# Optimization experiments

Measured on AMD Instinct MI355X. Metric: run time of the kernel, lower is better.

Reference implementation:

```python
import jax, jax.numpy as jnp
import numpy as np

B, S, E, H = 4, 1024, 1024, 16
HD = E // H  # head_dim = 64


def setup_inputs() -> dict:
    key = jax.random.key(0)
    ks = jax.random.split(key, 7)
    return {
        "query": jax.random.normal(ks[0], (B, S, E), dtype=jnp.float32),
        "key": jax.random.normal(ks[1], (B, S, E), dtype=jnp.float32),
        "value": jax.random.normal(ks[2], (B, S, E), dtype=jnp.float32),
        # per-head Linear weights stacked: [H, head_dim, emb_dim] (torch Linear is y = x @ W^T)
        "Wq": jax.random.normal(ks[3], (H, HD, E), dtype=jnp.float32) * (E ** -0.5),
        "Wk": jax.random.normal(ks[4], (H, HD, E), dtype=jnp.float32) * (E ** -0.5),
        "Wv": jax.random.normal(ks[5], (H, HD, E), dtype=jnp.float32) * (E ** -0.5),
        "Wo": jax.random.normal(ks[6], (E, E), dtype=jnp.float32) * (E ** -0.5),
    }


def reference(query, key, value, Wq, Wk, Wv, Wo):
    # Project per head (all heads vectorized): [B,S,E] x [H,HD,E] -> [B,H,S,HD]
    Q = jnp.einsum('bse,hde->bhsd', query, Wq)
    K = jnp.einsum('bse,hde->bhsd', key, Wk)
    V = jnp.einsum('bse,hde->bhsd', value, Wv)
    scale = 1.0 / np.sqrt(HD)  # source divides by sqrt(emb_dim / n_head)
    scores = jnp.einsum('bhsd,bhtd->bhst', Q, K) * scale  # [B,H,S,S]
    p = jax.nn.softmax(scores, axis=-1)
    ctx = jnp.einsum('bhst,bhtd->bhsd', p, V)  # [B,H,S,HD]
    # concat heads along feature dim -> [B,S,E]
    concat = ctx.transpose(0, 2, 1, 3).reshape(query.shape[0], query.shape[1], -1)
    return concat @ Wo.T
```

## Files before the change

### kernel.cpp

```cpp
#include <hip/hip_runtime.h>

typedef __bf16 bf16_t;
typedef __bf16 bf16x4 __attribute__((ext_vector_type(4)));
typedef __bf16 bf16x8 __attribute__((ext_vector_type(8)));
typedef float f32x4 __attribute__((ext_vector_type(4)));
typedef short short4v __attribute__((ext_vector_type(4)));

#define E_DIM 1024
#define S_LEN 1024
#define NHEAD 16
#define HD_DIM 64
#define BATCH 4
#define TOKENS 4096

__device__ __forceinline__ void async_copy16(const bf16_t* g, bf16_t* l) {
    __builtin_amdgcn_global_load_lds((const __attribute__((address_space(1))) void*)g,
                                     (__attribute__((address_space(3))) void*)l,
                                     16, 0, 0);
}

__device__ __forceinline__ f32x4 pv_mfma(bf16x4 a, bf16x4 b, f32x4 c) {
#if __has_builtin(__builtin_amdgcn_mfma_f32_16x16x16_bf16)
    return __builtin_amdgcn_mfma_f32_16x16x16_bf16(a, b, c, 0, 0, 0);
#elif __has_builtin(__builtin_amdgcn_mfma_f32_16x16x16bf16_1k)
    short4v as, bs;
    __builtin_memcpy(&as, &a, 8);
    __builtin_memcpy(&bs, &b, 8);
    return __builtin_amdgcn_mfma_f32_16x16x16bf16_1k(as, bs, c, 0, 0, 0);
#else
    f32x4 d;
    asm volatile("v_mfma_f32_16x16x16_bf16 %0, %1, %2, %3\n\ts_nop 7\n\ts_nop 7"
                 : "=v"(d)
                 : "v"(a), "v"(b), "v"(c));
    return d;
#endif
}

__device__ __forceinline__ void stage_tiles(const bf16_t* gA, const bf16_t* gB,
                                            bf16_t* sAbuf, bf16_t* sBbuf,
                                            int wave, int k0) {
    const int K = 1024;
#pragma unroll
    for (int cc = 0; cc < 4; cc++) {
        int c = wave * 4 + cc;
        if (c < 8)
            async_copy16(gA + (size_t)c * 16 * K + k0, sAbuf + c * 16 * 32);
        else
            async_copy16(gB + (size_t)(c - 8) * 16 * K + k0, sBbuf + (c - 8) * 16 * 32);
    }
}

__global__ __launch_bounds__(256) void cast_all(const float* __restrict__ q,
                                                const float* __restrict__ k,
                                                const float* __restrict__ v,
                                                const float* __restrict__ wq,
                                                const float* __restrict__ wk,
                                                const float* __restrict__ wv,
                                                const float* __restrict__ wo,
                                                bf16_t* __restrict__ dst) {
    const size_t NX = (size_t)TOKENS * E_DIM;
    const size_t NW = (size_t)E_DIM * E_DIM;
    size_t i = ((size_t)blockIdx.x * 256 + threadIdx.x) * 8;
    const float* src;
    size_t off;
    if (i < 3 * NX) {
        int a = (int)(i >> 22);
        src = a == 0 ? q : (a == 1 ? k : v);
        off = i & (NX - 1);
    } else {
        size_t j = i - 3 * NX;
        int a = (int)(j >> 20);
        src = a == 0 ? wq : (a == 1 ? wk : (a == 2 ? wv : wo));
        off = j & (NW - 1);
    }
    float4 x = *(const float4*)(src + off);
    float4 y = *(const float4*)(src + off + 4);
    bf16x8 o;
    o[0] = (bf16_t)x.x; o[1] = (bf16_t)x.y; o[2] = (bf16_t)x.z; o[3] = (bf16_t)x.w;
    o[4] = (bf16_t)y.x; o[5] = (bf16_t)y.y; o[6] = (bf16_t)y.z; o[7] = (bf16_t)y.w;
    *(bf16x8*)(dst + i) = o;
}

__global__ __launch_bounds__(256, 4) void proj_gemm(const bf16_t* __restrict__ Xq,
                                                    const bf16_t* __restrict__ Xk,
                                                    const bf16_t* __restrict__ Xv,
                                                    const bf16_t* __restrict__ Wq,
                                                    const bf16_t* __restrict__ Wk,
                                                    const bf16_t* __restrict__ Wv,
                                                    bf16_t* __restrict__ Qp,
                                                    bf16_t* __restrict__ Kp,
                                                    bf16_t* __restrict__ Vp) {
    __shared__ bf16_t sA[2][128 * 32];
    __shared__ bf16_t sB[2][128 * 32];
    const int z = blockIdx.z;
    const bf16_t* A = z == 0 ? Xq : (z == 1 ? Xk : Xv);
    const bf16_t* B = z == 0 ? Wq : (z == 1 ? Wk : Wv);
    bf16_t* C = z == 0 ? Qp : (z == 1 ? Kp : Vp);
    const int N = 1024, K = 1024;
    const int lid = blockIdx.x + 8 * blockIdx.y;
    const int m0 = (((lid & 7) << 2) + ((lid >> 3) & 3)) * 128;
    const int n0 = (lid >> 5) * 128;

    const int tid = threadIdx.x;
    const int wave = tid >> 6, lane = tid & 63;
    const int quad = lane >> 4, l16 = lane & 15;
    const int wm = (wave >> 1) * 64, wn = (wave & 1) * 64;
    const int srow = lane >> 2, scol = (lane & 3) * 8;

    const bf16_t* gA = A + (size_t)(m0 + srow) * K + scol;
    const bf16_t* gB = B + (size_t)(n0 + srow) * K + scol;

    f32x4 acc[4][4];
    const f32x4 vzero = {0.f, 0.f, 0.f, 0.f};
#pragma unroll
    for (int mt = 0; mt < 4; mt++)
#pragma unroll
        for (int nt = 0; nt < 4; nt++) acc[mt][nt] = vzero;

#define PROJ_COMPUTE(cur)                                                             \
    {                                                                                 \
        bf16x8 af[4], bfr[4];                                                         \
        _Pragma("unroll") for (int mt = 0; mt < 4; mt++)                              \
            af[mt] = *(const bf16x8*)&sA[cur][(wm + mt * 16 + l16) * 32 + quad * 8];  \
        _Pragma("unroll") for (int nt = 0; nt < 4; nt++)                              \
            bfr[nt] = *(const bf16x8*)&sB[cur][(wn + nt * 16 + l16) * 32 + quad * 8]; \
        _Pragma("unroll") for (int mt = 0; mt < 4; mt++)                              \
            _Pragma("unroll") for (int nt = 0; nt < 4; nt++)                          \
                acc[mt][nt] = __builtin_amdgcn_mfma_f32_16x16x32_bf16(                \
                    af[mt], bfr[nt], acc[mt][nt], 0, 0, 0);                           \
    }

    stage_tiles(gA, gB, sA[0], sB[0], wave, 0);
    stage_tiles(gA, gB, sA[1], sB[1], wave, 32);

    int cur = 0;
#pragma unroll 1
    for (int it = 0; it < 31; ++it) {
        asm volatile("s_waitcnt vmcnt(4)" ::: "memory");
        asm volatile("s_barrier" ::: "memory");
        PROJ_COMPUTE(cur);
        asm volatile("s_waitcnt lgkmcnt(0)" ::: "memory");
        asm volatile("s_barrier" ::: "memory");
        int knext = (it + 2) * 32;
        if (knext < K) stage_tiles(gA, gB, sA[cur], sB[cur], wave, knext);
        cur ^= 1;
    }
    asm volatile("s_waitcnt vmcnt(0)" ::: "memory");
    asm volatile("s_barrier" ::: "memory");
    PROJ_COMPUTE(cur);
#undef PROJ_COMPUTE

#pragma unroll
    for (int mt = 0; mt < 4; mt++)
#pragma unroll
        for (int nt = 0; nt < 4; nt++)
#pragma unroll
            for (int r = 0; r < 4; r++) {
                int row = m0 + wm + mt * 16 + quad * 4 + r;
                int col = n0 + wn + nt * 16 + l16;
                C[(size_t)row * N + col] = (bf16_t)acc[mt][nt][r];
            }
}

__global__ __launch_bounds__(256, 4) void out_gemm(const bf16_t* __restrict__ A,
                                                   const bf16_t* __restrict__ B,
                                                   float* __restrict__ C) {
    __shared__ bf16_t sA[2][128 * 32];
    __shared__ bf16_t sB[2][128 * 32];
    const int N = 1024, K = 1024;
    const int lid = blockIdx.x + 8 * blockIdx.y;
    const int m0 = (((lid & 7) << 2) + ((lid >> 3) & 3)) * 128;
    const int n0 = (lid >> 5) * 128;

    const int tid = threadIdx.x;
    const int wave = tid >> 6, lane = tid & 63;
    const int quad = lane >> 4, l16 = lane & 15;
    const int wm = (wave >> 1) * 64, wn = (wave & 1) * 64;
    const int srow = lane >> 2, scol = (lane & 3) * 8;

    const bf16_t* gA = A + (size_t)(m0 + srow) * K + scol;
    const bf16_t* gB = B + (size_t)(n0 + srow) * K + scol;

    f32x4 acc[4][4];
    const f32x4 vzero = {0.f, 0.f, 0.f, 0.f};
#pragma unroll
    for (int mt = 0; mt < 4; mt++)
#pragma unroll
        for (int nt = 0; nt < 4; nt++) acc[mt][nt] = vzero;

    stage_tiles(gA, gB, sA[0], sB[0], wave, 0);
    asm volatile("s_waitcnt vmcnt(0)" ::: "memory");
    __syncthreads();

    int cur = 0;
    for (int k0 = 32; k0 < K; k0 += 32) {
        stage_tiles(gA, gB, sA[cur ^ 1], sB[cur ^ 1], wave, k0);

        bf16x8 af[4], bfr[4];
#pragma unroll
        for (int mt = 0; mt < 4; mt++)
            af[mt] = *(const bf16x8*)&sA[cur][(wm + mt * 16 + l16) * 32 + quad * 8];
#pragma unroll
        for (int nt = 0; nt < 4; nt++)
            bfr[nt] = *(const bf16x8*)&sB[cur][(wn + nt * 16 + l16) * 32 + quad * 8];
#pragma unroll
        for (int mt = 0; mt < 4; mt++)
#pragma unroll
            for (int nt = 0; nt < 4; nt++)
                acc[mt][nt] = __builtin_amdgcn_mfma_f32_16x16x32_bf16(af[mt], bfr[nt],
                                                                      acc[mt][nt], 0, 0, 0);

        asm volatile("s_waitcnt vmcnt(0)" ::: "memory");
        __syncthreads();
        cur ^= 1;
    }

    {
        bf16x8 af[4], bfr[4];
#pragma unroll
        for (int mt = 0; mt < 4; mt++)
            af[mt] = *(const bf16x8*)&sA[cur][(wm + mt * 16 + l16) * 32 + quad * 8];
#pragma unroll
        for (int nt = 0; nt < 4; nt++)
            bfr[nt] = *(const bf16x8*)&sB[cur][(wn + nt * 16 + l16) * 32 + quad * 8];
#pragma unroll
        for (int mt = 0; mt < 4; mt++)
#pragma unroll
            for (int nt = 0; nt < 4; nt++)
                acc[mt][nt] = __builtin_amdgcn_mfma_f32_16x16x32_bf16(af[mt], bfr[nt],
                                                                      acc[mt][nt], 0, 0, 0);
    }

#pragma unroll
    for (int mt = 0; mt < 4; mt++)
#pragma unroll
        for (int nt = 0; nt < 4; nt++)
#pragma unroll
            for (int r = 0; r < 4; r++) {
                int row = m0 + wm + mt * 16 + quad * 4 + r;
                int col = n0 + wn + nt * 16 + l16;
                C[(size_t)row * N + col] = acc[mt][nt][r];
            }
}

#define KP 72

__global__ __launch_bounds__(256, 2) void flash_attn(const bf16_t* __restrict__ Q,
                                                     const bf16_t* __restrict__ K,
                                                     const bf16_t* __restrict__ V,
                                                     bf16_t* __restrict__ O) {
    __shared__ bf16_t smem[2 * 64 * KP];
    bf16_t* sK = smem;
    bf16_t* sVt = smem + 64 * KP;

    const int tid = threadIdx.x;
    const int wave = tid >> 6, lane = tid & 63;
    const int quad = lane >> 4, l16 = lane & 15;
    const int qt = blockIdx.y >> 1;
    const int h = blockIdx.x * 2 + (blockIdx.y & 1);
    const int b = blockIdx.z;
    const size_t base = (size_t)b * S_LEN * E_DIM + h * HD_DIM;
    const float c_exp = 0.125f * 1.44269504089f;

    bf16x8 qf[2][2];
#pragma unroll
    for (int mt = 0; mt < 2; mt++) {
        const bf16_t* qp =
            Q + base + (size_t)(qt * 128 + wave * 32 + mt * 16 + l16) * E_DIM + quad * 8;
        qf[mt][0] = *(const bf16x8*)qp;
        qf[mt][1] = *(const bf16x8*)(qp + 32);
    }

    float lsum[2] = {0.f, 0.f};
    f32x4 acc[2][4];
    const f32x4 vzero = {0.f, 0.f, 0.f, 0.f};
#pragma unroll
    for (int mt = 0; mt < 2; mt++)
#pragma unroll
        for (int dt = 0; dt < 4; dt++) acc[mt][dt] = vzero;

    const int stg = tid & 7;

    for (int j0 = 0; j0 < S_LEN; j0 += 64) {
        __syncthreads();
#pragma unroll
        for (int it = 0; it < 2; it++) {
            int r = (tid >> 3) + it * 32;
            int c = stg * 8;
            bf16x8 kv = *(const bf16x8*)(K + base + (size_t)(j0 + r) * E_DIM + c);
            *(bf16x8*)&sK[r * KP + c] = kv;
            bf16x8 vv = *(const bf16x8*)(V + base + (size_t)(j0 + r) * E_DIM + c);
            int jb = (((r >> 2) ^ stg) << 2) | (r & 3);
#pragma unroll
            for (int i = 0; i < 8; i++) sVt[(c + i) * KP + jb] = vv[i];
        }
        __syncthreads();

        bf16x8 kf[4][2];
#pragma unroll
        for (int jt = 0; jt < 4; jt++) {
            kf[jt][0] = *(const bf16x8*)&sK[(jt * 16 + l16) * KP + quad * 8];
            kf[jt][1] = *(const bf16x8*)&sK[(jt * 16 + l16) * KP + 32 + quad * 8];
        }

        bf16x4 pb[2][4];
#pragma unroll
        for (int mt = 0; mt < 2; mt++)
#pragma unroll
            for (int jt = 0; jt < 4; jt++) {
                f32x4 s = vzero;
                s = __builtin_amdgcn_mfma_f32_16x16x32_bf16(kf[jt][0], qf[mt][0], s, 0, 0, 0);
                s = __builtin_amdgcn_mfma_f32_16x16x32_bf16(kf[jt][1], qf[mt][1], s, 0, 0, 0);
#pragma unroll
                for (int r = 0; r < 4; r++) {
                    float p = __builtin_amdgcn_exp2f(s[r] * c_exp);
                    lsum[mt] += p;
                    pb[mt][jt][r] = (bf16_t)p;
                }
            }

#pragma unroll
        for (int jt = 0; jt < 4; jt++)
#pragma unroll
            for (int dt = 0; dt < 4; dt++) {
                int cidx = (jt * 4 + quad) ^ (dt * 2 + (l16 >> 3));
                bf16x4 vf = *(const bf16x4*)&sVt[(dt * 16 + l16) * KP + cidx * 4];
#pragma unroll
                for (int mt = 0; mt < 2; mt++)
                    acc[mt][dt] = pv_mfma(vf, pb[mt][jt], acc[mt][dt]);
            }
    }

    float inv[2];
#pragma unroll
    for (int mt = 0; mt < 2; mt++) {
        lsum[mt] += __shfl_xor(lsum[mt], 16);
        lsum[mt] += __shfl_xor(lsum[mt], 32);
        inv[mt] = __builtin_amdgcn_rcpf(lsum[mt]);
    }

    __syncthreads();
    bf16_t* ep = smem + wave * 32 * KP;
#pragma unroll
    for (int mt = 0; mt < 2; mt++)
#pragma unroll
        for (int dt = 0; dt < 4; dt++)
#pragma unroll
            for (int r = 0; r < 4; r++)
                ep[(mt * 16 + l16) * KP + dt * 16 + quad * 4 + r] =
                    (bf16_t)(acc[mt][dt][r] * inv[mt]);
#pragma unroll
    for (int mt = 0; mt < 2; mt++)
#pragma unroll
        for (int c = 0; c < 2; c++) {
            int row = lane >> 2;
            int col = (lane & 3) * 8 + c * 32;
            bf16x8 oval = *(const bf16x8*)&ep[(mt * 16 + row) * KP + col];
            *(bf16x8*)&O[base + (size_t)(qt * 128 + wave * 32 + mt * 16 + row) * E_DIM + col] =
                oval;
        }
}

extern "C" void kernel_launch(void* const* d_in, const int* in_sizes, int n_in,
                              void* d_out, int out_size, void* d_ws, size_t ws_size,
                              hipStream_t stream) {
    const float* q  = (const float*)d_in[0];
    const float* k  = (const float*)d_in[1];
    const float* v  = (const float*)d_in[2];
    const float* wq = (const float*)d_in[3];
    const float* wk = (const float*)d_in[4];
    const float* wv = (const float*)d_in[5];
    const float* wo = (const float*)d_in[6];
    float* out = (float*)d_out;

    const int NX = TOKENS * E_DIM;
    const int NW = E_DIM * E_DIM;

    bf16_t* ws  = (bf16_t*)d_ws;
    bf16_t* Xq  = ws;
    bf16_t* Xk  = ws + (size_t)NX;
    bf16_t* Xv  = ws + (size_t)2 * NX;
    bf16_t* Wqb = ws + (size_t)3 * NX;
    bf16_t* Wkb = Wqb + NW;
    bf16_t* Wvb = Wkb + NW;
    bf16_t* Wob = Wvb + NW;
    bf16_t* Qp  = Wob + NW;
    bf16_t* Kp  = Qp + (size_t)NX;
    bf16_t* Vp  = Kp + (size_t)NX;
    bf16_t* ctx = Xq;

    cast_all<<<8192, 256, 0, stream>>>(q, k, v, wq, wk, wv, wo, Xq);

    proj_gemm<<<dim3(8, 32, 3), 256, 0, stream>>>(Xq, Xk, Xv, Wqb, Wkb, Wvb, Qp, Kp, Vp);

    flash_attn<<<dim3(8, 16, 4), 256, 0, stream>>>(Qp, Kp, Vp, ctx);

    out_gemm<<<dim3(8, 32), 256, 0, stream>>>(ctx, Wob, out);
}
```

Measured before the change: 188.9 us.

## Deepen GEMM prefetch and double-buffer K/V tiles in flash attention

The output-projection GEMM now issues two stages of async global-to-LDS copies up front and waits with a partial vmcnt, so the load for tile k+2 overlaps compute on tile k instead of draining all loads each iteration. The flash attention kernel gains a second LDS buffer and register prefetch of the next K/V tile, writing it to the alternate buffer after the MFMAs so global latency hides behind compute and one barrier per iteration is removed. This doubles attention LDS use, which may limit occupancy at launch bounds of 2 blocks, and the hand-placed waitcnt/barrier sequencing assumes K=1024 (31 iterations hard-coded).

```diff
diff --git a/kernel.cpp b/kernel.cpp
--- a/kernel.cpp
+++ b/kernel.cpp
@@ -188,48 +188,38 @@
 #pragma unroll
         for (int nt = 0; nt < 4; nt++) acc[mt][nt] = vzero;
 
+#define OUT_COMPUTE(cur)                                                              \
+    {                                                                                 \
+        bf16x8 af[4], bfr[4];                                                         \
+        _Pragma("unroll") for (int mt = 0; mt < 4; mt++)                              \
+            af[mt] = *(const bf16x8*)&sA[cur][(wm + mt * 16 + l16) * 32 + quad * 8];  \
+        _Pragma("unroll") for (int nt = 0; nt < 4; nt++)                              \
+            bfr[nt] = *(const bf16x8*)&sB[cur][(wn + nt * 16 + l16) * 32 + quad * 8]; \
+        _Pragma("unroll") for (int mt = 0; mt < 4; mt++)                              \
+            _Pragma("unroll") for (int nt = 0; nt < 4; nt++)                          \
+                acc[mt][nt] = __builtin_amdgcn_mfma_f32_16x16x32_bf16(                \
+                    af[mt], bfr[nt], acc[mt][nt], 0, 0, 0);                           \
+    }
+
     stage_tiles(gA, gB, sA[0], sB[0], wave, 0);
+    stage_tiles(gA, gB, sA[1], sB[1], wave, 32);
+
+    int cur = 0;
+#pragma unroll 1
+    for (int it = 0; it < 31; ++it) {
+        asm volatile("s_waitcnt vmcnt(4)" ::: "memory");
+        asm volatile("s_barrier" ::: "memory");
+        OUT_COMPUTE(cur);
+        asm volatile("s_waitcnt lgkmcnt(0)" ::: "memory");
+        asm volatile("s_barrier" ::: "memory");
+        int knext = (it + 2) * 32;
+        if (knext < K) stage_tiles(gA, gB, sA[cur], sB[cur], wave, knext);
+        cur ^= 1;
+    }
     asm volatile("s_waitcnt vmcnt(0)" ::: "memory");
-    __syncthreads();
-
-    int cur = 0;
-    for (int k0 = 32; k0 < K; k0 += 32) {
-        stage_tiles(gA, gB, sA[cur ^ 1], sB[cur ^ 1], wave, k0);
-
-        bf16x8 af[4], bfr[4];
-#pragma unroll
-        for (int mt = 0; mt < 4; mt++)
-            af[mt] = *(const bf16x8*)&sA[cur][(wm + mt * 16 + l16) * 32 + quad * 8];
-#pragma unroll
-        for (int nt = 0; nt < 4; nt++)
-            bfr[nt] = *(const bf16x8*)&sB[cur][(wn + nt * 16 + l16) * 32 + quad * 8];
-#pragma unroll
-        for (int mt = 0; mt < 4; mt++)
-#pragma unroll
-            for (int nt = 0; nt < 4; nt++)
-                acc[mt][nt] = __builtin_amdgcn_mfma_f32_16x16x32_bf16(af[mt], bfr[nt],
-                                                                      acc[mt][nt], 0, 0, 0);
-
-        asm volatile("s_waitcnt vmcnt(0)" ::: "memory");
-        __syncthreads();
-        cur ^= 1;
-    }
-
-    {
-        bf16x8 af[4], bfr[4];
-#pragma unroll
-        for (int mt = 0; mt < 4; mt++)
-            af[mt] = *(const bf16x8*)&sA[cur][(wm + mt * 16 + l16) * 32 + quad * 8];
-#pragma unroll
-        for (int nt = 0; nt < 4; nt++)
-            bfr[nt] = *(const bf16x8*)&sB[cur][(wn + nt * 16 + l16) * 32 + quad * 8];
-#pragma unroll
-        for (int mt = 0; mt < 4; mt++)
-#pragma unroll
-            for (int nt = 0; nt < 4; nt++)
-                acc[mt][nt] = __builtin_amdgcn_mfma_f32_16x16x32_bf16(af[mt], bfr[nt],
-                                                                      acc[mt][nt], 0, 0, 0);
-    }
+    asm volatile("s_barrier" ::: "memory");
+    OUT_COMPUTE(cur);
+#undef OUT_COMPUTE
 
 #pragma unroll
     for (int mt = 0; mt < 4; mt++)
@@ -249,9 +239,7 @@
                                                      const bf16_t* __restrict__ K,
                                                      const bf16_t* __restrict__ V,
                                                      bf16_t* __restrict__ O) {
-    __shared__ bf16_t smem[2 * 64 * KP];
-    bf16_t* sK = smem;
-    bf16_t* sVt = smem + 64 * KP;
+    __shared__ bf16_t smem[2][2 * 64 * KP];
 
     const int tid = threadIdx.x;
     const int wave = tid >> 6, lane = tid & 63;
@@ -280,21 +268,43 @@
         for (int dt = 0; dt < 4; dt++) acc[mt][dt] = vzero;
 
     const int stg = tid & 7;
-
+    const int r0 = tid >> 3;
+    const int c0 = stg * 8;
+    const bf16_t* Kbase = K + base + (size_t)r0 * E_DIM + c0;
+    const bf16_t* Vbase = V + base + (size_t)r0 * E_DIM + c0;
+
+    bf16x8 kvn[2], vvn[2];
+#pragma unroll
+    for (int it = 0; it < 2; it++) {
+        kvn[it] = *(const bf16x8*)(Kbase + (size_t)it * 32 * E_DIM);
+        vvn[it] = *(const bf16x8*)(Vbase + (size_t)it * 32 * E_DIM);
+    }
+    {
+        bf16_t* dK = smem[0];
+        bf16_t* dVt = smem[0] + 64 * KP;
+#pragma unroll
+        for (int it = 0; it < 2; it++) {
+            int r = r0 + it * 32;
+            *(bf16x8*)&dK[r * KP + c0] = kvn[it];
+            int jb = (((r >> 2) ^ stg) << 2) | (r & 3);
+#pragma unroll
+            for (int i = 0; i < 8; i++) dVt[(c0 + i) * KP + jb] = vvn[it][i];
+        }
+    }
+
+    int cur = 0;
     for (int j0 = 0; j0 < S_LEN; j0 += 64) {
-        __syncthreads();
-#pragma unroll
-        for (int it = 0; it < 2; it++) {
-            int r = (tid >> 3) + it * 32;
-            int c = stg * 8;
-            bf16x8 kv = *(const bf16x8*)(K + base + (size_t)(j0 + r) * E_DIM + c);
-            *(bf16x8*)&sK[r * KP + c] = kv;
-            bf16x8 vv = *(const bf16x8*)(V + base + (size_t)(j0 + r) * E_DIM + c);
-            int jb = (((r >> 2) ^ stg) << 2) | (r & 3);
-#pragma unroll
-            for (int i = 0; i < 8; i++) sVt[(c + i) * KP + jb] = vv[i];
+        const bool more = (j0 + 64 < S_LEN);
+        if (more) {
+#pragma unroll
+            for (int it = 0; it < 2; it++) {
+                kvn[it] = *(const bf16x8*)(Kbase + (size_t)(j0 + 64 + it * 32) * E_DIM);
+                vvn[it] = *(const bf16x8*)(Vbase + (size_t)(j0 + 64 + it * 32) * E_DIM);
+            }
         }
         __syncthreads();
+        const bf16_t* sK = smem[cur];
+        const bf16_t* sVt = smem[cur] + 64 * KP;
 
         bf16x8 kf[4][2];
 #pragma unroll
@@ -329,6 +339,20 @@
                 for (int mt = 0; mt < 2; mt++)
                     acc[mt][dt] = pv_mfma(vf, pb[mt][jt], acc[mt][dt]);
             }
+
+        if (more) {
+            bf16_t* dK = smem[cur ^ 1];
+            bf16_t* dVt = smem[cur ^ 1] + 64 * KP;
+#pragma unroll
+            for (int it = 0; it < 2; it++) {
+                int r = r0 + it * 32;
+                *(bf16x8*)&dK[r * KP + c0] = kvn[it];
+                int jb = (((r >> 2) ^ stg) << 2) | (r & 3);
+#pragma unroll
+                for (int i = 0; i < 8; i++) dVt[(c0 + i) * KP + jb] = vvn[it][i];
+            }
+        }
+        cur ^= 1;
     }
 
     float inv[2];
@@ -340,7 +364,7 @@
     }
 
     __syncthreads();
-    bf16_t* ep = smem + wave * 32 * KP;
+    bf16_t* ep = smem[0] + wave * 32 * KP;
 #pragma unroll
     for (int mt = 0; mt < 2; mt++)
 #pragma unroll
```

Measured after the change: 189.2 us. About the same (+0.2%).

## Triple-buffer LDS tiles in projection and output GEMMs

Applied to the files above, without the earlier changes.

Both GEMM kernels move from double to triple buffering of their LDS tiles, keeping two k-tiles of global-to-LDS async loads in flight while the current tile is computed. The output GEMM also drops its single-stage vmcnt(0) wait per iteration in favour of the same waitcnt/barrier schedule the projection GEMM uses. The aim is to hide more global memory latency. In exchange, LDS per block goes from 32KB to 48KB and the occupancy hint drops from 4 to 3 blocks per CU.

```diff
diff --git a/kernel.cpp b/kernel.cpp
--- a/kernel.cpp
+++ b/kernel.cpp
@@ -81,7 +81,7 @@
     *(bf16x8*)(dst + i) = o;
 }
 
-__global__ __launch_bounds__(256, 4) void proj_gemm(const bf16_t* __restrict__ Xq,
+__global__ __launch_bounds__(256, 3) void proj_gemm(const bf16_t* __restrict__ Xq,
                                                     const bf16_t* __restrict__ Xk,
                                                     const bf16_t* __restrict__ Xv,
                                                     const bf16_t* __restrict__ Wq,
@@ -90,8 +90,8 @@
                                                     bf16_t* __restrict__ Qp,
                                                     bf16_t* __restrict__ Kp,
                                                     bf16_t* __restrict__ Vp) {
-    __shared__ bf16_t sA[2][128 * 32];
-    __shared__ bf16_t sB[2][128 * 32];
+    __shared__ bf16_t sA[3][128 * 32];
+    __shared__ bf16_t sB[3][128 * 32];
     const int z = blockIdx.z;
     const bf16_t* A = z == 0 ? Xq : (z == 1 ? Xk : Xv);
     const bf16_t* B = z == 0 ? Wq : (z == 1 ? Wk : Wv);
@@ -132,19 +132,27 @@
 
     stage_tiles(gA, gB, sA[0], sB[0], wave, 0);
     stage_tiles(gA, gB, sA[1], sB[1], wave, 32);
+    stage_tiles(gA, gB, sA[2], sB[2], wave, 64);
 
     int cur = 0;
 #pragma unroll 1
-    for (int it = 0; it < 31; ++it) {
-        asm volatile("s_waitcnt vmcnt(4)" ::: "memory");
+    for (int it = 0; it < 29; ++it) {
+        asm volatile("s_waitcnt vmcnt(8)" ::: "memory");
         asm volatile("s_barrier" ::: "memory");
         PROJ_COMPUTE(cur);
         asm volatile("s_waitcnt lgkmcnt(0)" ::: "memory");
         asm volatile("s_barrier" ::: "memory");
-        int knext = (it + 2) * 32;
-        if (knext < K) stage_tiles(gA, gB, sA[cur], sB[cur], wave, knext);
-        cur ^= 1;
-    }
+        stage_tiles(gA, gB, sA[cur], sB[cur], wave, (it + 3) * 32);
+        cur = cur == 2 ? 0 : cur + 1;
+    }
+    asm volatile("s_waitcnt vmcnt(8)" ::: "memory");
+    asm volatile("s_barrier" ::: "memory");
+    PROJ_COMPUTE(cur);
+    cur = cur == 2 ? 0 : cur + 1;
+    asm volatile("s_waitcnt vmcnt(4)" ::: "memory");
+    asm volatile("s_barrier" ::: "memory");
+    PROJ_COMPUTE(cur);
+    cur = cur == 2 ? 0 : cur + 1;
     asm volatile("s_waitcnt vmcnt(0)" ::: "memory");
     asm volatile("s_barrier" ::: "memory");
     PROJ_COMPUTE(cur);
@@ -162,11 +170,11 @@
             }
 }
 
-__global__ __launch_bounds__(256, 4) void out_gemm(const bf16_t* __restrict__ A,
+__global__ __launch_bounds__(256, 3) void out_gemm(const bf16_t* __restrict__ A,
                                                    const bf16_t* __restrict__ B,
                                                    float* __restrict__ C) {
-    __shared__ bf16_t sA[2][128 * 32];
-    __shared__ bf16_t sB[2][128 * 32];
+    __shared__ bf16_t sA[3][128 * 32];
+    __shared__ bf16_t sB[3][128 * 32];
     const int N = 1024, K = 1024;
     const int lid = blockIdx.x + 8 * blockIdx.y;
     const int m0 = (((lid & 7) << 2) + ((lid >> 3) & 3)) * 128;
@@ -188,48 +196,46 @@
 #pragma unroll
         for (int nt = 0; nt < 4; nt++) acc[mt][nt] = vzero;
 
+#define OUT_COMPUTE(cur)                                                              \
+    {                                                                                 \
+        bf16x8 af[4], bfr[4];                                                         \
+        _Pragma("unroll") for (int mt = 0; mt < 4; mt++)                              \
+            af[mt] = *(const bf16x8*)&sA[cur][(wm + mt * 16 + l16) * 32 + quad * 8];  \
+        _Pragma("unroll") for (int nt = 0; nt < 4; nt++)                              \
+            bfr[nt] = *(const bf16x8*)&sB[cur][(wn + nt * 16 + l16) * 32 + quad * 8]; \
+        _Pragma("unroll") for (int mt = 0; mt < 4; mt++)                              \
+            _Pragma("unroll") for (int nt = 0; nt < 4; nt++)                          \
+                acc[mt][nt] = __builtin_amdgcn_mfma_f32_16x16x32_bf16(                \
+                    af[mt], bfr[nt], acc[mt][nt], 0, 0, 0);                           \
+    }
+
     stage_tiles(gA, gB, sA[0], sB[0], wave, 0);
+    stage_tiles(gA, gB, sA[1], sB[1], wave, 32);
+    stage_tiles(gA, gB, sA[2], sB[2], wave, 64);
+
+    int cur = 0;
+#pragma unroll 1
+    for (int it = 0; it < 29; ++it) {
+        asm volatile("s_waitcnt vmcnt(8)" ::: "memory");
+        asm volatile("s_barrier" ::: "memory");
+        OUT_COMPUTE(cur);
+        asm volatile("s_waitcnt lgkmcnt(0)" ::: "memory");
+        asm volatile("s_barrier" ::: "memory");
+        stage_tiles(gA, gB, sA[cur], sB[cur], wave, (it + 3) * 32);
+        cur = cur == 2 ? 0 : cur + 1;
+    }
+    asm volatile("s_waitcnt vmcnt(8)" ::: "memory");
+    asm volatile("s_barrier" ::: "memory");
+    OUT_COMPUTE(cur);
+    cur = cur == 2 ? 0 : cur + 1;
+    asm volatile("s_waitcnt vmcnt(4)" ::: "memory");
+    asm volatile("s_barrier" ::: "memory");
+    OUT_COMPUTE(cur);
+    cur = cur == 2 ? 0 : cur + 1;
     asm volatile("s_waitcnt vmcnt(0)" ::: "memory");
-    __syncthreads();
-
-    int cur = 0;
-    for (int k0 = 32; k0 < K; k0 += 32) {
-        stage_tiles(gA, gB, sA[cur ^ 1], sB[cur ^ 1], wave, k0);
-
-        bf16x8 af[4], bfr[4];
-#pragma unroll
-        for (int mt = 0; mt < 4; mt++)
-            af[mt] = *(const bf16x8*)&sA[cur][(wm + mt * 16 + l16) * 32 + quad * 8];
-#pragma unroll
-        for (int nt = 0; nt < 4; nt++)
-            bfr[nt] = *(const bf16x8*)&sB[cur][(wn + nt * 16 + l16) * 32 + quad * 8];
-#pragma unroll
-        for (int mt = 0; mt < 4; mt++)
-#pragma unroll
-            for (int nt = 0; nt < 4; nt++)
-                acc[mt][nt] = __builtin_amdgcn_mfma_f32_16x16x32_bf16(af[mt], bfr[nt],
-                                                                      acc[mt][nt], 0, 0, 0);
-
-        asm volatile("s_waitcnt vmcnt(0)" ::: "memory");
-        __syncthreads();
-        cur ^= 1;
-    }
-
-    {
-        bf16x8 af[4], bfr[4];
-#pragma unroll
-        for (int mt = 0; mt < 4; mt++)
-            af[mt] = *(const bf16x8*)&sA[cur][(wm + mt * 16 + l16) * 32 + quad * 8];
-#pragma unroll
-        for (int nt = 0; nt < 4; nt++)
-            bfr[nt] = *(const bf16x8*)&sB[cur][(wn + nt * 16 + l16) * 32 + quad * 8];
-#pragma unroll
-        for (int mt = 0; mt < 4; mt++)
-#pragma unroll
-            for (int nt = 0; nt < 4; nt++)
-                acc[mt][nt] = __builtin_amdgcn_mfma_f32_16x16x32_bf16(af[mt], bfr[nt],
-                                                                      acc[mt][nt], 0, 0, 0);
-    }
+    asm volatile("s_barrier" ::: "memory");
+    OUT_COMPUTE(cur);
+#undef OUT_COMPUTE
 
 #pragma unroll
     for (int mt = 0; mt < 4; mt++)
```

Result: no change. 185.9 us (-1.6%).
